# Optimization experiments

Measured on AMD Instinct MI355X. Metric: run time of the kernel, lower is better.

## Reference

```python
import jax, jax.numpy as jnp
import numpy as np

N_NODES = 20000
N_EDGES = 200000
N_GRAPHS = 128
EMB = 256
N_LAYERS = 4
NUM_ELEMENTS = 84
RBF_DIM = 10
RBF_CUTOFF = 8.0


def setup_inputs() -> dict:
    key = jax.random.key(0)
    ks = jax.random.split(key, 20)
    inp = {
        'x': jax.random.randint(ks[0], (N_NODES, 1), 0, NUM_ELEMENTS, dtype=jnp.int64) if jax.config.read('jax_enable_x64') else jax.random.randint(ks[0], (N_NODES, 1), 0, NUM_ELEMENTS).astype(jnp.int32),
        'src': jax.random.randint(ks[1], (N_EDGES,), 0, N_NODES).astype(jnp.int32),
        'dst': jax.random.randint(ks[2], (N_EDGES,), 0, N_NODES).astype(jnp.int32),
        'e': jax.random.uniform(ks[3], (N_EDGES, 1), dtype=jnp.float32) * RBF_CUTOFF,
        'i': jnp.sort(jax.random.randint(ks[4], (N_NODES,), 0, N_GRAPHS)).astype(jnp.int32),
    }
    s_emb = 1.0 / np.sqrt(EMB)
    # element embedding table
    inp['emb_table'] = jax.random.normal(ks[5], (NUM_ELEMENTS, EMB), jnp.float32) * s_emb
    # dense_e applied to RBF expansion
    inp['We'] = jax.random.normal(ks[6], (RBF_DIM, EMB), jnp.float32) * (1.0 / np.sqrt(RBF_DIM))
    inp['be'] = jnp.zeros((EMB,), jnp.float32)
    # CGCNN-style gated message passing layers (stacked over layers)
    def w(k):
        return jax.random.normal(k, (N_LAYERS, EMB, EMB), jnp.float32) * s_emb
    inp['Wg_x'] = w(ks[7]); inp['Wg_n'] = w(ks[8]); inp['Wg_e'] = w(ks[9])
    inp['bg'] = jnp.zeros((N_LAYERS, EMB), jnp.float32)
    inp['Wf_x'] = w(ks[10]); inp['Wf_n'] = w(ks[11]); inp['Wf_e'] = w(ks[12])
    inp['bf'] = jnp.zeros((N_LAYERS, EMB), jnp.float32)
    # dense_n: embedding -> 12
    inp['Wn'] = jax.random.normal(ks[13], (EMB, 12), jnp.float32) * s_emb
    inp['bn'] = jnp.zeros((12,), jnp.float32)
    return inp


def _rbf_expand(d):
    # Gaussian radial basis expansion of scalar distances: [E] -> [E, RBF_DIM]
    centers = jnp.linspace(0.0, RBF_CUTOFF, RBF_DIM, dtype=d.dtype)
    width = centers[1] - centers[0]
    return jnp.exp(-(((d[:, None] - centers) / width) ** 2))


def reference(x, src, dst, e, i, emb_table, We, be, Wg_x, Wg_n, Wg_e, bg,
              Wf_x, Wf_n, Wf_e, bf, Wn, bn):
    xn = emb_table[x[:, 0]]                     # [N, EMB] element embedding
    ef = _rbf_expand(e[:, 0]) @ We + be         # [E, EMB] edge features
    for l in range(N_LAYERS):
        h_i = xn[dst]                           # receiver node features [E, EMB]
        h_j = xn[src]                           # sender node features   [E, EMB]
        # gate/filter computed as split matmuls (equivalent to Dense on concat)
        zg = h_i @ Wg_x[l] + h_j @ Wg_n[l] + ef @ Wg_e[l] + bg[l]
        zf = h_i @ Wf_x[l] + h_j @ Wf_n[l] + ef @ Wf_e[l] + bf[l]
        msg = jax.nn.sigmoid(zg) * jax.nn.softplus(zf)   # [E, EMB]
        agg = jax.ops.segment_sum(msg, dst, num_segments=N_NODES)
        xn = agg + xn                           # residual add (in model call)
    xs = xn @ Wn + bn                           # [N, 12]
    sums = jax.ops.segment_sum(xs, i, num_segments=N_GRAPHS)
    cnts = jax.ops.segment_sum(jnp.ones((xs.shape[0], 1), xs.dtype), i,
                               num_segments=N_GRAPHS)
    out = sums / jnp.maximum(cnts, 1.0)         # global average pool per graph
    return out.reshape(N_GRAPHS, 3, 4)
```

## Files before the change

kernel.cpp:

```cpp
#include <hip/hip_runtime.h>
#include <hip/hip_bf16.h>
#include <math.h>

#define NN   20000
#define NE   200000
#define NG   128
#define EMBD 256
#define NL   4
#define RBFD 10
#define GSPL 8

typedef __attribute__((ext_vector_type(8))) short bf16x8;
typedef __attribute__((ext_vector_type(4))) float f32x4;
typedef __attribute__((ext_vector_type(2))) float f32x2;

__device__ __forceinline__ f32x2 mk2(float a, float b) { f32x2 r; r.x = a; r.y = b; return r; }
__device__ __forceinline__ f32x2 bfpair(unsigned u) {
  return mk2(__uint_as_float(u << 16), __uint_as_float(u & 0xffff0000u));
}


__global__ void k_embed(const int* __restrict__ x, const float* __restrict__ emb,
                        float* __restrict__ xn, __hip_bfloat16* __restrict__ xnb) {
  int idx = blockIdx.x * blockDim.x + threadIdx.x;
  if (idx >= NN * (EMBD / 4)) return;
  int n  = idx >> 6;
  int c4 = (idx & 63) << 2;
  float4 v = *(const float4*)(emb + (size_t)x[n] * EMBD + c4);
  *(float4*)(xn + (size_t)n * EMBD + c4) = v;
  __hip_bfloat16* xb = xnb + (size_t)n * EMBD + c4;
  xb[0] = __float2bfloat16(v.x); xb[1] = __float2bfloat16(v.y);
  xb[2] = __float2bfloat16(v.z); xb[3] = __float2bfloat16(v.w);
}

__global__ void k_wsmall(const float* __restrict__ We, const float* __restrict__ be,
                         const float* __restrict__ Wge, const float* __restrict__ bg,
                         const float* __restrict__ Wfe, const float* __restrict__ bf,
                         float* __restrict__ weff, float* __restrict__ beff) {
  int tid = blockIdx.x * blockDim.x + threadIdx.x;
  const int WPER = RBFD * EMBD;
  if (tid < NL * 2 * WPER) {
    int l  = tid / (2 * WPER);
    int r  = tid % (2 * WPER);
    int gf = r / WPER;
    int r2 = r % WPER;
    int k = r2 / EMBD, c = r2 % EMBD;
    const float* W = (gf == 0 ? Wge : Wfe) + (size_t)l * EMBD * EMBD;
    float s = 0.f;
    for (int j = 0; j < EMBD; ++j) s += We[k * EMBD + j] * W[(size_t)j * EMBD + c];
    weff[tid] = s;
  } else {
    int t2 = tid - NL * 2 * WPER;
    if (t2 >= NL * 2 * EMBD) return;
    int l  = t2 / (2 * EMBD);
    int r  = t2 % (2 * EMBD);
    int gf = r / EMBD, c = r % EMBD;
    const float* W = (gf == 0 ? Wge : Wfe) + (size_t)l * EMBD * EMBD;
    const float* b = (gf == 0 ? bg : bf) + (size_t)l * EMBD;
    float s = b[c];
    for (int j = 0; j < EMBD; ++j) s += be[j] * W[(size_t)j * EMBD + c];
    beff[t2] = s;
  }
}

__global__ __launch_bounds__(256) void k_wprep(
    const float* __restrict__ Wgx, const float* __restrict__ Wfx,
    const float* __restrict__ Wgn, const float* __restrict__ Wfn,
    __hip_bfloat16* __restrict__ WT) {
  __shared__ float T[64][65];
  int lq = blockIdx.x; int l = lq >> 2, q = lq & 3;
  const float* W = (q == 0 ? Wgx : q == 1 ? Wfx : q == 2 ? Wgn : Wfn) + (size_t)l * 65536;
  int t = blockIdx.y;
  int k0 = (t & 3) * 64, c0 = (t >> 2) * 64;
  #pragma unroll
  for (int i = 0; i < 16; ++i) {
    int idx = threadIdx.x + i * 256;
    int r = idx >> 6, c = idx & 63;
    T[r][c] = W[(size_t)(k0 + r) * 256 + c0 + c];
  }
  __syncthreads();
  __hip_bfloat16* out = WT + ((size_t)lq * 256) * 256;
  #pragma unroll
  for (int i = 0; i < 16; ++i) {
    int idx = threadIdx.x + i * 256;
    int r = idx >> 6, c = idx & 63;
    out[(size_t)(c0 + r) * 256 + k0 + c] = __float2bfloat16(T[c][r]);
  }
}


__global__ void k_hist(const int* __restrict__ dst, int* __restrict__ cnt) {
  int e = blockIdx.x * blockDim.x + threadIdx.x;
  if (e >= NE) return;
  atomicAdd(&cnt[dst[e]], 1);
}

__global__ __launch_bounds__(1024) void k_scan(const int* __restrict__ cnt,
                                               int* __restrict__ roff,
                                               int* __restrict__ cursor) {
  __shared__ int part[1024];
  const int t = threadIdx.x;
  const int CH = 20;
  int base = t * CH;
  int loc[CH];
  int s = 0;
  #pragma unroll
  for (int i = 0; i < CH; ++i) {
    int idx = base + i;
    int v = (idx < NN) ? cnt[idx] : 0;
    loc[i] = s;
    s += v;
  }
  part[t] = s;
  __syncthreads();
  for (int off = 1; off < 1024; off <<= 1) {
    int v = (t >= off) ? part[t - off] : 0;
    __syncthreads();
    part[t] += v;
    __syncthreads();
  }
  int chunkbase = (t == 0) ? 0 : part[t - 1];
  #pragma unroll
  for (int i = 0; i < CH; ++i) {
    int idx = base + i;
    if (idx < NN) {
      int v = chunkbase + loc[i];
      roff[idx] = v;
      cursor[idx] = v;
    }
  }
  if (t == 1023) roff[NN] = part[1023];
}

__global__ void k_scatter(const int* __restrict__ src, const int* __restrict__ dst,
                          const float* __restrict__ edist,
                          int* __restrict__ cursor,
                          int* __restrict__ src_s, float* __restrict__ rbf_s) {
  int e = blockIdx.x * blockDim.x + threadIdx.x;
  if (e >= NE) return;
  int d = dst[e];
  int p = atomicAdd(&cursor[d], 1);
  src_s[p] = src[e];
  float dd = edist[e];
  const float width = 8.0f / 9.0f;
  #pragma unroll
  for (int k = 0; k < RBFD; ++k) {
    float t = (dd - (float)k * width) / width;
    rbf_s[(size_t)p * RBFD + k] = __expf(-t * t);
  }
}


__global__ __launch_bounds__(256) void k_nodemm(
    const __hip_bfloat16* __restrict__ xnb, const __hip_bfloat16* __restrict__ WTl,
    float* __restrict__ Y, __hip_bfloat16* __restrict__ Yb) {
  __shared__ unsigned short As[128 * 32];
  __shared__ unsigned short Bs[128 * 32];
  const int tid = threadIdx.x;
  const int lane = tid & 63;
  const int wave = tid >> 6;
  const int row0 = blockIdx.x << 7;
  const int by = blockIdx.y;
  const int col0 = by << 7;
  const int q = col0 >> 8;
  const int cb = col0 & 255;
  const unsigned short* xb = (const unsigned short*)xnb;
  const unsigned short* Wb = (const unsigned short*)WTl + ((size_t)q * 256 + cb) * 256;
  const int wr = (wave >> 1) << 6;
  const int wc = (wave & 1) << 6;
  f32x4 acc[4][4] = {};

  for (int k0 = 0; k0 < 256; k0 += 32) {
    #pragma unroll
    for (int h = 0; h < 2; ++h) {
      int c = tid + (h << 8);
      int r = c >> 2, s = c & 3;
      int sw = s ^ ((r >> 1) & 3);
      int ga = row0 + r; if (ga > NN - 1) ga = NN - 1;
      *(bf16x8*)(&As[r * 32 + sw * 8]) =
          *(const bf16x8*)(xb + (size_t)ga * 256 + k0 + s * 8);
      *(bf16x8*)(&Bs[r * 32 + sw * 8]) =
          *(const bf16x8*)(Wb + (size_t)r * 256 + k0 + s * 8);
    }
    __syncthreads();
    bf16x8 af[4], bfr[4];
    const int rsel = lane & 15, ksl = lane >> 4;
    #pragma unroll
    for (int m = 0; m < 4; ++m) {
      int r = wr + m * 16 + rsel;
      int sw = ksl ^ ((r >> 1) & 3);
      af[m] = *(const bf16x8*)(&As[r * 32 + sw * 8]);
    }
    #pragma unroll
    for (int n = 0; n < 4; ++n) {
      int r = wc + n * 16 + rsel;
      int sw = ksl ^ ((r >> 1) & 3);
      bfr[n] = *(const bf16x8*)(&Bs[r * 32 + sw * 8]);
    }
    #pragma unroll
    for (int m = 0; m < 4; ++m)
      #pragma unroll
      for (int n = 0; n < 4; ++n)
        acc[m][n] = __builtin_amdgcn_mfma_f32_16x16x32_bf16(af[m], bfr[n], acc[m][n], 0, 0, 0);
    __syncthreads();
  }

  const int crow = (lane >> 4) << 2;
  const int ccol = lane & 15;
  if (by < 4) {
    #pragma unroll
    for (int m = 0; m < 4; ++m)
      #pragma unroll
      for (int j = 0; j < 4; ++j) {
        int gr = row0 + wr + m * 16 + crow + j;
        if (gr < NN) {
          #pragma unroll
          for (int n = 0; n < 4; ++n)
            Y[(size_t)gr * 512 + col0 + wc + n * 16 + ccol] = acc[m][n][j];
        }
      }
  } else {
    const int dcol = col0 - 512;
    #pragma unroll
    for (int m = 0; m < 4; ++m)
      #pragma unroll
      for (int j = 0; j < 4; ++j) {
        int gr = row0 + wr + m * 16 + crow + j;
        if (gr < NN) {
          #pragma unroll
          for (int n = 0; n < 4; ++n)
            Yb[(size_t)gr * 512 + dcol + wc + n * 16 + ccol] = __float2bfloat16(acc[m][n][j]);
        }
      }
  }
}

__device__ __forceinline__ float fast_sigmoid(float z) {
  return __builtin_amdgcn_rcpf(1.0f + __expf(-z));
}
__device__ __forceinline__ float fast_softplus(float z) {
  return fmaxf(z, 0.0f) + __logf(1.0f + __expf(-fabsf(z)));
}

__global__ __launch_bounds__(256, 4) void k_agg(
    const float* __restrict__ Y, const __hip_bfloat16* __restrict__ Yb,
    const int* __restrict__ roff,
    const int* __restrict__ src_s, const float* __restrict__ rbf_s,
    const float* __restrict__ weff, const float* __restrict__ beff,
    float* __restrict__ xn, __hip_bfloat16* __restrict__ xnb, int layer) {
  __shared__ float WgS[RBFD * EMBD];
  __shared__ float WfS[RBFD * EMBD];
  __shared__ float bS[2 * EMBD];
  const int tid = threadIdx.x;
  const float* wbase = weff + (size_t)layer * 2 * RBFD * EMBD;
  for (int i = tid; i < RBFD * EMBD; i += 256) {
    WgS[i] = wbase[i];
    WfS[i] = wbase[RBFD * EMBD + i];
  }
  for (int i = tid; i < 2 * EMBD; i += 256) bS[i] = beff[(size_t)layer * 2 * EMBD + i];
  __syncthreads();
  const int wave = tid >> 6, lane = tid & 63;
  const int c4 = lane << 2;
  const int n = blockIdx.x * 4 + wave;
  if (n >= NN) return;
  const int deg = roff[n + 1] - roff[n];
  const int jb = __builtin_amdgcn_readfirstlane(roff[n]);

  f32x2 wg0[RBFD], wg1[RBFD], wf0[RBFD], wf1[RBFD];
  #pragma unroll
  for (int k = 0; k < RBFD; ++k) {
    float4 g4 = *(const float4*)&WgS[k * EMBD + c4];
    float4 f4 = *(const float4*)&WfS[k * EMBD + c4];
    wg0[k] = mk2(g4.x, g4.y); wg1[k] = mk2(g4.z, g4.w);
    wf0[k] = mk2(f4.x, f4.y); wf1[k] = mk2(f4.z, f4.w);
  }

  const float4 bg4 = *(const float4*)&bS[c4];
  const float4 bf4 = *(const float4*)&bS[EMBD + c4];
  const float4 Ax = *(const float4*)(Y + (size_t)n * 512 + c4);
  const float4 Fx = *(const float4*)(Y + (size_t)n * 512 + 256 + c4);
  const f32x2 bg0 = mk2(Ax.x + bg4.x, Ax.y + bg4.y);
  const f32x2 bg1 = mk2(Ax.z + bg4.z, Ax.w + bg4.w);
  const f32x2 bf0 = mk2(Fx.x + bf4.x, Fx.y + bf4.y);
  const f32x2 bf1 = mk2(Fx.z + bf4.z, Fx.w + bf4.w);

  f32x2 macc0 = mk2(0.f, 0.f), macc1 = mk2(0.f, 0.f);
  if (deg > 0) {
    const unsigned short* Ybp = (const unsigned short*)Yb + c4;
    int scur = src_s[jb];
    uint2 pa = *(const uint2*)(Ybp + (size_t)scur * 512);
    uint2 pf = *(const uint2*)(Ybp + (size_t)scur * 512 + 256);
    for (int i = 0; i < deg; ++i) {
      uint2 na = pa, nf = pf;
      if (i + 1 < deg) {
        int sn = src_s[jb + i + 1];
        na = *(const uint2*)(Ybp + (size_t)sn * 512);
        nf = *(const uint2*)(Ybp + (size_t)sn * 512 + 256);
      }
      const float* rp = rbf_s + (size_t)(jb + i) * RBFD;
      f32x2 zg0 = bg0 + bfpair(pa.x);
      f32x2 zg1 = bg1 + bfpair(pa.y);
      f32x2 zf0 = bf0 + bfpair(pf.x);
      f32x2 zf1 = bf1 + bfpair(pf.y);
      #pragma unroll
      for (int k = 0; k < RBFD; ++k) {
        float rk = rp[k];
        zg0 += rk * wg0[k]; zg1 += rk * wg1[k];
        zf0 += rk * wf0[k]; zf1 += rk * wf1[k];
      }
      macc0.x += fast_sigmoid(zg0.x) * fast_softplus(zf0.x);
      macc0.y += fast_sigmoid(zg0.y) * fast_softplus(zf0.y);
      macc1.x += fast_sigmoid(zg1.x) * fast_softplus(zf1.x);
      macc1.y += fast_sigmoid(zg1.y) * fast_softplus(zf1.y);
      pa = na; pf = nf;
    }
  }
  float4 xv = *(const float4*)(xn + (size_t)n * EMBD + c4);
  xv.x += macc0.x; xv.y += macc0.y; xv.z += macc1.x; xv.w += macc1.y;
  *(float4*)(xn + (size_t)n * EMBD + c4) = xv;
  __hip_bfloat16* xbp = xnb + (size_t)n * EMBD + c4;
  xbp[0] = __float2bfloat16(xv.x); xbp[1] = __float2bfloat16(xv.y);
  xbp[2] = __float2bfloat16(xv.z); xbp[3] = __float2bfloat16(xv.w);
}


__global__ __launch_bounds__(256) void k_gsum(
    const float* __restrict__ xn, const int* __restrict__ gi,
    float* __restrict__ gpart, float* __restrict__ gcnt) {
  const int g = blockIdx.x, p = blockIdx.y;
  int lo = 0, hi = NN;
  while (lo < hi) { int m = (lo + hi) >> 1; if (gi[m] < g) lo = m + 1; else hi = m; }
  int lo2 = lo, hi2 = NN;
  while (lo2 < hi2) { int m = (lo2 + hi2) >> 1; if (gi[m] < g + 1) lo2 = m + 1; else hi2 = m; }
  const int cntv = lo2 - lo;
  const int r0 = lo + (cntv * p) / GSPL;
  const int r1 = lo + (cntv * (p + 1)) / GSPL;
  const int c = threadIdx.x;
  float acc = 0.f;
  for (int r = r0; r < r1; ++r) acc += xn[(size_t)r * EMBD + c];
  gpart[((size_t)g * GSPL + p) * EMBD + c] = acc;
  if (p == 0 && c == 0) gcnt[g] = (float)cntv;
}

__global__ __launch_bounds__(256) void k_final(
    const float* __restrict__ gpart, const float* __restrict__ gcnt,
    const float* __restrict__ Wn, const float* __restrict__ bn,
    float* __restrict__ out) {
  __shared__ float s[EMBD];
  const int g = blockIdx.x;
  const int c = threadIdx.x;
  float v = 0.f;
  #pragma unroll
  for (int p = 0; p < GSPL; ++p) v += gpart[((size_t)g * GSPL + p) * EMBD + c];
  s[c] = v;
  __syncthreads();
  if (c < 12) {
    float acc = 0.f;
    for (int k = 0; k < EMBD; ++k) acc += s[k] * Wn[k * 12 + c];
    float cv = gcnt[g];
    out[g * 12 + c] = (cv > 0.f) ? acc / cv + bn[c] : 0.f;
  }
}


extern "C" void kernel_launch(void* const* d_in, const int* in_sizes, int n_in,
                              void* d_out, int out_size, void* d_ws, size_t ws_size,
                              hipStream_t stream) {
  const int*   x   = (const int*)d_in[0];
  const int*   src = (const int*)d_in[1];
  const int*   dst = (const int*)d_in[2];
  const float* e   = (const float*)d_in[3];
  const int*   gi  = (const int*)d_in[4];
  const float* emb = (const float*)d_in[5];
  const float* We  = (const float*)d_in[6];
  const float* be  = (const float*)d_in[7];
  const float* Wgx = (const float*)d_in[8];
  const float* Wgn = (const float*)d_in[9];
  const float* Wge = (const float*)d_in[10];
  const float* bg  = (const float*)d_in[11];
  const float* Wfx = (const float*)d_in[12];
  const float* Wfn = (const float*)d_in[13];
  const float* Wfe = (const float*)d_in[14];
  const float* bf  = (const float*)d_in[15];
  const float* Wn  = (const float*)d_in[16];
  const float* bn  = (const float*)d_in[17];
  float* out = (float*)d_out;

  char* ws = (char*)d_ws;
  size_t off = 0;
  auto alloc = [&](size_t bytes) {
    void* p = ws + off;
    off += (bytes + 255) & ~(size_t)255;
    return p;
  };
  float*           xn    = (float*)alloc((size_t)NN * EMBD * 4);
  __hip_bfloat16*  xnb   = (__hip_bfloat16*)alloc((size_t)NN * EMBD * 2);
  float*           Y     = (float*)alloc((size_t)NN * 512 * 4);
  __hip_bfloat16*  Yb    = (__hip_bfloat16*)alloc((size_t)NN * 512 * 2);
  float*           rbf_s = (float*)alloc((size_t)NE * RBFD * 4);
  int*             src_s = (int*)alloc((size_t)NE * 4);
  int*             cnt   = (int*)alloc((size_t)NN * 4);
  int*             roff  = (int*)alloc((size_t)(NN + 1) * 4);
  int*             curs  = (int*)alloc((size_t)NN * 4);
  float*           weff  = (float*)alloc((size_t)NL * 2 * RBFD * EMBD * 4);
  float*           beff  = (float*)alloc((size_t)NL * 2 * EMBD * 4);
  __hip_bfloat16*  WT    = (__hip_bfloat16*)alloc((size_t)NL * 4 * 256 * 256 * 2);
  float*           gpart = (float*)alloc((size_t)NG * GSPL * EMBD * 4);
  float*           gcnt  = (float*)alloc((size_t)NG * 4);
  (void)ws_size; (void)in_sizes; (void)n_in; (void)out_size;

  hipMemsetAsync(cnt, 0, (size_t)NN * 4, stream);

  k_embed<<<(NN * (EMBD / 4) + 255) / 256, 256, 0, stream>>>(x, emb, xn, xnb);
  k_wsmall<<<(NL * 2 * (RBFD + 1) * EMBD + 255) / 256, 256, 0, stream>>>(
      We, be, Wge, bg, Wfe, bf, weff, beff);
  k_wprep<<<dim3(NL * 4, 16), 256, 0, stream>>>(Wgx, Wfx, Wgn, Wfn, WT);
  k_hist<<<(NE + 255) / 256, 256, 0, stream>>>(dst, cnt);
  k_scan<<<1, 1024, 0, stream>>>(cnt, roff, curs);
  k_scatter<<<(NE + 255) / 256, 256, 0, stream>>>(src, dst, e, curs, src_s, rbf_s);

  dim3 mmgrid((NN + 127) / 128, 8);
  for (int l = 0; l < NL; ++l) {
    k_nodemm<<<mmgrid, 256, 0, stream>>>(xnb, WT + (size_t)l * 4 * 65536, Y, Yb);
    k_agg<<<(NN + 3) / 4, 256, 0, stream>>>(Y, Yb, roff, src_s, rbf_s, weff, beff, xn, xnb, l);
  }
  k_gsum<<<dim3(NG, GSPL), 256, 0, stream>>>(xn, gi, gpart, gcnt);
  k_final<<<NG, 256, 0, stream>>>(gpart, gcnt, Wn, bn, out);
}
```

Before: 550.4 us.

## Store all node-matmul outputs as bf16 and vectorize edge loads in aggregation

The node GEMM now writes all 1024 output columns as one interleaved bf16 buffer instead of a separate fp32 receiver part, which roughly halves that write and the per-node read. RBF rows are padded to 12 floats so they load as vectors and are prefetched along with the next neighbour's features. Each wave loads up to 64 source indices once and broadcasts them with shuffles. The per-block LDS copy of the RBF weights is replaced by direct global loads into registers, with occupancy lowered to 3 blocks. Rounding the receiver-side terms to bf16 reduces precision, and the larger register footprint may limit latency hiding.

```diff
diff --git a/kernel.cpp b/kernel.cpp
--- a/kernel.cpp
+++ b/kernel.cpp
@@ -8,15 +8,20 @@
 #define EMBD 256
 #define NL   4
 #define RBFD 10
+#define RBFP 12
 #define GSPL 8
 
 typedef __attribute__((ext_vector_type(8))) short bf16x8;
 typedef __attribute__((ext_vector_type(4))) float f32x4;
 typedef __attribute__((ext_vector_type(2))) float f32x2;
 
-__device__ __forceinline__ f32x2 mk2(float a, float b) { f32x2 r; r.x = a; r.y = b; return r; }
-__device__ __forceinline__ f32x2 bfpair(unsigned u) {
-  return mk2(__uint_as_float(u << 16), __uint_as_float(u & 0xffff0000u));
+__device__ __forceinline__ f32x4 unpk(uint2 u) {
+  f32x4 r;
+  r.x = __uint_as_float(u.x << 16);
+  r.y = __uint_as_float(u.x & 0xffff0000u);
+  r.z = __uint_as_float(u.y << 16);
+  r.w = __uint_as_float(u.y & 0xffff0000u);
+  return r;
 }
 
 
@@ -143,17 +148,22 @@
   src_s[p] = src[e];
   float dd = edist[e];
   const float width = 8.0f / 9.0f;
+  float r[RBFD];
   #pragma unroll
   for (int k = 0; k < RBFD; ++k) {
     float t = (dd - (float)k * width) / width;
-    rbf_s[(size_t)p * RBFD + k] = __expf(-t * t);
-  }
+    r[k] = __expf(-t * t);
+  }
+  float* rp = rbf_s + (size_t)p * RBFP;
+  *(float4*)(rp + 0) = make_float4(r[0], r[1], r[2], r[3]);
+  *(float4*)(rp + 4) = make_float4(r[4], r[5], r[6], r[7]);
+  *(float4*)(rp + 8) = make_float4(r[8], r[9], 0.f, 0.f);
 }
 
 
 __global__ __launch_bounds__(256) void k_nodemm(
     const __hip_bfloat16* __restrict__ xnb, const __hip_bfloat16* __restrict__ WTl,
-    float* __restrict__ Y, __hip_bfloat16* __restrict__ Yb) {
+    __hip_bfloat16* __restrict__ Yb) {
   __shared__ unsigned short As[128 * 32];
   __shared__ unsigned short Bs[128 * 32];
   const int tid = threadIdx.x;
@@ -207,32 +217,17 @@
 
   const int crow = (lane >> 4) << 2;
   const int ccol = lane & 15;
-  if (by < 4) {
+  #pragma unroll
+  for (int m = 0; m < 4; ++m)
     #pragma unroll
-    for (int m = 0; m < 4; ++m)
-      #pragma unroll
-      for (int j = 0; j < 4; ++j) {
-        int gr = row0 + wr + m * 16 + crow + j;
-        if (gr < NN) {
-          #pragma unroll
-          for (int n = 0; n < 4; ++n)
-            Y[(size_t)gr * 512 + col0 + wc + n * 16 + ccol] = acc[m][n][j];
-        }
+    for (int j = 0; j < 4; ++j) {
+      int gr = row0 + wr + m * 16 + crow + j;
+      if (gr < NN) {
+        #pragma unroll
+        for (int n = 0; n < 4; ++n)
+          Yb[(size_t)gr * 1024 + col0 + wc + n * 16 + ccol] = __float2bfloat16(acc[m][n][j]);
       }
-  } else {
-    const int dcol = col0 - 512;
-    #pragma unroll
-    for (int m = 0; m < 4; ++m)
-      #pragma unroll
-      for (int j = 0; j < 4; ++j) {
-        int gr = row0 + wr + m * 16 + crow + j;
-        if (gr < NN) {
-          #pragma unroll
-          for (int n = 0; n < 4; ++n)
-            Yb[(size_t)gr * 512 + dcol + wc + n * 16 + ccol] = __float2bfloat16(acc[m][n][j]);
-        }
-      }
-  }
+    }
 }
 
 __device__ __forceinline__ float fast_sigmoid(float z) {
@@ -242,81 +237,78 @@
   return fmaxf(z, 0.0f) + __logf(1.0f + __expf(-fabsf(z)));
 }
 
-__global__ __launch_bounds__(256, 4) void k_agg(
-    const float* __restrict__ Y, const __hip_bfloat16* __restrict__ Yb,
-    const int* __restrict__ roff,
+__global__ __launch_bounds__(256, 3) void k_agg(
+    const __hip_bfloat16* __restrict__ Yb, const int* __restrict__ roff,
     const int* __restrict__ src_s, const float* __restrict__ rbf_s,
     const float* __restrict__ weff, const float* __restrict__ beff,
     float* __restrict__ xn, __hip_bfloat16* __restrict__ xnb, int layer) {
-  __shared__ float WgS[RBFD * EMBD];
-  __shared__ float WfS[RBFD * EMBD];
-  __shared__ float bS[2 * EMBD];
-  const int tid = threadIdx.x;
-  const float* wbase = weff + (size_t)layer * 2 * RBFD * EMBD;
-  for (int i = tid; i < RBFD * EMBD; i += 256) {
-    WgS[i] = wbase[i];
-    WfS[i] = wbase[RBFD * EMBD + i];
-  }
-  for (int i = tid; i < 2 * EMBD; i += 256) bS[i] = beff[(size_t)layer * 2 * EMBD + i];
-  __syncthreads();
-  const int wave = tid >> 6, lane = tid & 63;
+  const int wave = threadIdx.x >> 6, lane = threadIdx.x & 63;
   const int c4 = lane << 2;
   const int n = blockIdx.x * 4 + wave;
   if (n >= NN) return;
-  const int deg = roff[n + 1] - roff[n];
   const int jb = __builtin_amdgcn_readfirstlane(roff[n]);
-
-  f32x2 wg0[RBFD], wg1[RBFD], wf0[RBFD], wf1[RBFD];
+  const int deg = roff[n + 1] - jb;
+
+  const float* wg_g = weff + (size_t)layer * 2 * RBFD * EMBD + c4;
+  const float* wf_g = wg_g + RBFD * EMBD;
+  f32x4 wg[RBFD], wf[RBFD];
   #pragma unroll
   for (int k = 0; k < RBFD; ++k) {
-    float4 g4 = *(const float4*)&WgS[k * EMBD + c4];
-    float4 f4 = *(const float4*)&WfS[k * EMBD + c4];
-    wg0[k] = mk2(g4.x, g4.y); wg1[k] = mk2(g4.z, g4.w);
-    wf0[k] = mk2(f4.x, f4.y); wf1[k] = mk2(f4.z, f4.w);
-  }
-
-  const float4 bg4 = *(const float4*)&bS[c4];
-  const float4 bf4 = *(const float4*)&bS[EMBD + c4];
-  const float4 Ax = *(const float4*)(Y + (size_t)n * 512 + c4);
-  const float4 Fx = *(const float4*)(Y + (size_t)n * 512 + 256 + c4);
-  const f32x2 bg0 = mk2(Ax.x + bg4.x, Ax.y + bg4.y);
-  const f32x2 bg1 = mk2(Ax.z + bg4.z, Ax.w + bg4.w);
-  const f32x2 bf0 = mk2(Fx.x + bf4.x, Fx.y + bf4.y);
-  const f32x2 bf1 = mk2(Fx.z + bf4.z, Fx.w + bf4.w);
-
-  f32x2 macc0 = mk2(0.f, 0.f), macc1 = mk2(0.f, 0.f);
+    wg[k] = *(const f32x4*)(wg_g + k * EMBD);
+    wf[k] = *(const f32x4*)(wf_g + k * EMBD);
+  }
+  const float* bb = beff + (size_t)layer * 2 * EMBD + c4;
+  f32x4 bgv = *(const f32x4*)(bb);
+  f32x4 bfv = *(const f32x4*)(bb + EMBD);
+
+  const unsigned short* yrow = (const unsigned short*)Yb + (size_t)n * 1024 + c4;
+  f32x4 bg = bgv + unpk(*(const uint2*)(yrow));
+  f32x4 bf = bfv + unpk(*(const uint2*)(yrow + 256));
+
+  f32x4 macc = {};
   if (deg > 0) {
-    const unsigned short* Ybp = (const unsigned short*)Yb + c4;
-    int scur = src_s[jb];
-    uint2 pa = *(const uint2*)(Ybp + (size_t)scur * 512);
-    uint2 pf = *(const uint2*)(Ybp + (size_t)scur * 512 + 256);
+    int sv = (lane < deg) ? src_s[jb + lane] : 0;
+    const unsigned short* Ysrc = (const unsigned short*)Yb + c4 + 512;
+    int s0 = __shfl(sv, 0, 64);
+    uint2 pa = *(const uint2*)(Ysrc + (size_t)s0 * 1024);
+    uint2 pf = *(const uint2*)(Ysrc + (size_t)s0 * 1024 + 256);
+    const float* rp0 = rbf_s + (size_t)jb * RBFP;
+    f32x4 r03 = *(const f32x4*)(rp0);
+    f32x4 r47 = *(const f32x4*)(rp0 + 4);
+    f32x2 r89 = *(const f32x2*)(rp0 + 8);
     for (int i = 0; i < deg; ++i) {
-      uint2 na = pa, nf = pf;
+      uint2 na = pa, nf2 = pf;
+      f32x4 n03 = r03, n47 = r47; f32x2 n89 = r89;
       if (i + 1 < deg) {
-        int sn = src_s[jb + i + 1];
-        na = *(const uint2*)(Ybp + (size_t)sn * 512);
-        nf = *(const uint2*)(Ybp + (size_t)sn * 512 + 256);
+        int sn = (i + 1 < 64) ? __shfl(sv, i + 1, 64) : src_s[jb + i + 1];
+        na  = *(const uint2*)(Ysrc + (size_t)sn * 1024);
+        nf2 = *(const uint2*)(Ysrc + (size_t)sn * 1024 + 256);
+        const float* rp = rbf_s + (size_t)(jb + i + 1) * RBFP;
+        n03 = *(const f32x4*)(rp);
+        n47 = *(const f32x4*)(rp + 4);
+        n89 = *(const f32x2*)(rp + 8);
       }
-      const float* rp = rbf_s + (size_t)(jb + i) * RBFD;
-      f32x2 zg0 = bg0 + bfpair(pa.x);
-      f32x2 zg1 = bg1 + bfpair(pa.y);
-      f32x2 zf0 = bf0 + bfpair(pf.x);
-      f32x2 zf1 = bf1 + bfpair(pf.y);
-      #pragma unroll
-      for (int k = 0; k < RBFD; ++k) {
-        float rk = rp[k];
-        zg0 += rk * wg0[k]; zg1 += rk * wg1[k];
-        zf0 += rk * wf0[k]; zf1 += rk * wf1[k];
-      }
-      macc0.x += fast_sigmoid(zg0.x) * fast_softplus(zf0.x);
-      macc0.y += fast_sigmoid(zg0.y) * fast_softplus(zf0.y);
-      macc1.x += fast_sigmoid(zg1.x) * fast_softplus(zf1.x);
-      macc1.y += fast_sigmoid(zg1.y) * fast_softplus(zf1.y);
-      pa = na; pf = nf;
+      f32x4 zg = bg + unpk(pa);
+      f32x4 zf = bf + unpk(pf);
+      zg += r03.x * wg[0]; zf += r03.x * wf[0];
+      zg += r03.y * wg[1]; zf += r03.y * wf[1];
+      zg += r03.z * wg[2]; zf += r03.z * wf[2];
+      zg += r03.w * wg[3]; zf += r03.w * wf[3];
+      zg += r47.x * wg[4]; zf += r47.x * wf[4];
+      zg += r47.y * wg[5]; zf += r47.y * wf[5];
+      zg += r47.z * wg[6]; zf += r47.z * wf[6];
+      zg += r47.w * wg[7]; zf += r47.w * wf[7];
+      zg += r89.x * wg[8]; zf += r89.x * wf[8];
+      zg += r89.y * wg[9]; zf += r89.y * wf[9];
+      macc.x += fast_sigmoid(zg.x) * fast_softplus(zf.x);
+      macc.y += fast_sigmoid(zg.y) * fast_softplus(zf.y);
+      macc.z += fast_sigmoid(zg.z) * fast_softplus(zf.z);
+      macc.w += fast_sigmoid(zg.w) * fast_softplus(zf.w);
+      pa = na; pf = nf2; r03 = n03; r47 = n47; r89 = n89;
     }
   }
   float4 xv = *(const float4*)(xn + (size_t)n * EMBD + c4);
-  xv.x += macc0.x; xv.y += macc0.y; xv.z += macc1.x; xv.w += macc1.y;
+  xv.x += macc.x; xv.y += macc.y; xv.z += macc.z; xv.w += macc.w;
   *(float4*)(xn + (size_t)n * EMBD + c4) = xv;
   __hip_bfloat16* xbp = xnb + (size_t)n * EMBD + c4;
   xbp[0] = __float2bfloat16(xv.x); xbp[1] = __float2bfloat16(xv.y);
@@ -395,9 +387,8 @@
   };
   float*           xn    = (float*)alloc((size_t)NN * EMBD * 4);
   __hip_bfloat16*  xnb   = (__hip_bfloat16*)alloc((size_t)NN * EMBD * 2);
-  float*           Y     = (float*)alloc((size_t)NN * 512 * 4);
-  __hip_bfloat16*  Yb    = (__hip_bfloat16*)alloc((size_t)NN * 512 * 2);
-  float*           rbf_s = (float*)alloc((size_t)NE * RBFD * 4);
+  __hip_bfloat16*  Yb    = (__hip_bfloat16*)alloc((size_t)NN * 1024 * 2);
+  float*           rbf_s = (float*)alloc((size_t)NE * RBFP * 4);
   int*             src_s = (int*)alloc((size_t)NE * 4);
   int*             cnt   = (int*)alloc((size_t)NN * 4);
   int*             roff  = (int*)alloc((size_t)(NN + 1) * 4);
@@ -421,8 +412,8 @@
 
   dim3 mmgrid((NN + 127) / 128, 8);
   for (int l = 0; l < NL; ++l) {
-    k_nodemm<<<mmgrid, 256, 0, stream>>>(xnb, WT + (size_t)l * 4 * 65536, Y, Yb);
-    k_agg<<<(NN + 3) / 4, 256, 0, stream>>>(Y, Yb, roff, src_s, rbf_s, weff, beff, xn, xnb, l);
+    k_nodemm<<<mmgrid, 256, 0, stream>>>(xnb, WT + (size_t)l * 4 * 65536, Yb);
+    k_agg<<<(NN + 3) / 4, 256, 0, stream>>>(Yb, roff, src_s, rbf_s, weff, beff, xn, xnb, l);
   }
   k_gsum<<<dim3(NG, GSPL), 256, 0, stream>>>(xn, gi, gpart, gcnt);
   k_final<<<NG, 256, 0, stream>>>(gpart, gcnt, Wn, bn, out);
```

Measured after the change: 567.1 us. 1.03x slower.
